# Performance work log

Measured on AMD Instinct MI355X. Metric: run time of the kernel, lower is better.

The kernel has to match this reference:

```python
import jax, jax.numpy as jnp
import numpy as np

N, T, F_IN, E, H, FW = 4096, 64, 8, 256, 512, 32
LN_EPS = 1e-5


def setup_inputs() -> dict:
    key = jax.random.key(0)
    ks = jax.random.split(key, 16)
    nrm = lambda k, s, sc=0.05: jax.random.normal(k, s, dtype=jnp.float32) * sc
    return {
        "x": nrm(ks[0], (N, T, F_IN), 1.0),
        "We": nrm(ks[1], (E, F_IN)), "be": nrm(ks[2], (E,)),
        "Wih0": nrm(ks[3], (4 * H, E)), "Whh0": nrm(ks[4], (4 * H, H)),
        "bih0": nrm(ks[5], (4 * H,)), "bhh0": nrm(ks[6], (4 * H,)),
        "Wih1": nrm(ks[7], (4 * H, H)), "Whh1": nrm(ks[8], (4 * H, H)),
        "bih1": nrm(ks[9], (4 * H,)), "bhh1": nrm(ks[10], (4 * H,)),
        "fc1_w": nrm(ks[11], (H, H)), "fc1_b": nrm(ks[12], (H,)),
        "ln_g": jnp.ones((H,), jnp.float32), "ln_b": jnp.zeros((H,), jnp.float32),
        "fc2_w": nrm(ks[13], (F_IN, H)), "fc2_b": nrm(ks[14], (F_IN,)),
    }


def _cell(x, h, c, Wih, Whh, bih, bhh):
    # PyTorch LSTM gate order: i, f, g, o
    g = x @ Wih.T + h @ Whh.T + (bih + bhh)
    i, f, gg, o = jnp.split(g, 4, axis=-1)
    c = jax.nn.sigmoid(f) * c + jax.nn.sigmoid(i) * jnp.tanh(gg)
    h = jax.nn.sigmoid(o) * jnp.tanh(c)
    return h, c


def _layer(xs, Wih, Whh, bih, bhh):
    # xs: (T, N, D) -> ys: (T, N, H), final (h, c)
    n = xs.shape[1]
    Hd = Whh.shape[1]
    h0 = jnp.zeros((n, Hd), xs.dtype)
    def step(carry, x_t):
        h, c = carry
        h, c = _cell(x_t, h, c, Wih, Whh, bih, bhh)
        return (h, c), h
    (h, c), ys = jax.lax.scan(step, (h0, h0), xs)
    return ys, h, c


def reference(x, We, be, Wih0, Whh0, bih0, bhh0, Wih1, Whh1, bih1, bhh1,
              fc1_w, fc1_b, ln_g, ln_b, fc2_w, fc2_b):
    x_enc = x[:, :-1, :]          # (N, T-1, F)
    x0 = x[:, -1, :]              # (N, F)

    # ---- encoder ----
    emb = x_enc @ We.T + be       # (N, T-1, E)
    xs = jnp.swapaxes(emb, 0, 1)  # (T-1, N, E)
    ys0, h0e, c0e = _layer(xs, Wih0, Whh0, bih0, bhh0)
    _, h1e, c1e = _layer(ys0, Wih1, Whh1, bih1, bhh1)

    # ---- decoder head: Linear -> LayerNorm -> ReLU -> Linear ----
    def fc(h):
        z = h @ fc1_w.T + fc1_b
        mu = z.mean(-1, keepdims=True)
        var = z.var(-1, keepdims=True)
        z = (z - mu) * jax.lax.rsqrt(var + LN_EPS) * ln_g + ln_b
        z = jax.nn.relu(z)
        return z @ fc2_w.T + fc2_b

    def dec_step(carry, _):
        xt, h0, c0, h1, c1 = carry
        e = xt @ We.T + be
        h0, c0 = _cell(e, h0, c0, Wih0, Whh0, bih0, bhh0)
        h1, c1 = _cell(h0, h1, c1, Wih1, Whh1, bih1, bhh1)
        y = fc(h1)
        return (y, h0, c0, h1, c1), y

    _, ys = jax.lax.scan(dec_step, (x0, h0e, c0e, h1e, c1e), None, length=FW)
    return jnp.swapaxes(ys, 0, 1)  # (N, FW, F)
```

## Files before the change

kernel.cpp:

```cpp
#include <hip/hip_runtime.h>
#include <math.h>

#define NB   4096
#define HID  512
#define G4H  2048
#define EDIM 256
#define FINP 8
#define TSTEPS 64
#define FWIN 32

typedef __bf16 bf16;
typedef bf16  bf16x8 __attribute__((ext_vector_type(8)));
typedef float f32x4  __attribute__((ext_vector_type(4)));

__device__ __forceinline__ float sigf(float x) { return 1.0f / (1.0f + __expf(-x)); }
__device__ __forceinline__ float tanhf_(float x) { return 2.0f * sigf(2.0f * x) - 1.0f; }

__device__ __forceinline__ void gload16(const void* g, void* l) {
    __builtin_amdgcn_global_load_lds((const __attribute__((address_space(1))) void*)g,
                                     (__attribute__((address_space(3))) void*)l, 16, 0, 0);
}

__device__ __forceinline__ void swz32(int& bx, int& by) {
    int nwg  = (int)(gridDim.x * gridDim.y);
    int orig = (int)(blockIdx.x + blockIdx.y * gridDim.x);
    int swz  = (orig & 7) * (nwg >> 3) + (orig >> 3);
    bx = swz & 31;
    by = swz >> 5;
}

__device__ __forceinline__ void gemm_acc(
    const bf16* __restrict__ A1, const bf16* __restrict__ W1,
    const bf16* __restrict__ A2, const bf16* __restrict__ W2, int npass,
    int m0, int n0, bf16 (&As)[2][4096], bf16 (&Ws)[2][4096], f32x4 (&acc)[4][4])
{
    const int tid  = threadIdx.x;
    const int lane = tid & 63;
    const int w    = tid >> 6;
    const int wr   = w >> 1, wc = w & 1;
    const int l16  = lane & 15;
    const int NK   = npass << 4;

    const int r0 = tid >> 2;
    const int o0 = ((tid & 3) ^ ((tid >> 3) & 3)) * 8;

    auto stage = [&](int s, int b) {
        const bf16* A = (s < 16) ? A1 : A2;
        const bf16* W = (s < 16) ? W1 : W2;
        const int k0 = ((s & 15) << 5) + o0;
        gload16(A + (size_t)(m0 + r0) * HID + k0,      &As[b][tid * 8]);
        gload16(A + (size_t)(m0 + r0 + 64) * HID + k0, &As[b][(tid + 256) * 8]);
        gload16(W + (size_t)(n0 + r0) * HID + k0,      &Ws[b][tid * 8]);
        gload16(W + (size_t)(n0 + r0 + 64) * HID + k0, &Ws[b][(tid + 256) * 8]);
    };

    const int swz_k = (((lane >> 4) ^ ((l16 >> 1) & 3))) * 8;
    const int aoff = wr * 2048 + l16 * 32 + swz_k;
    const int boff = wc * 2048 + l16 * 32 + swz_k;

    stage(0, 0);
    __syncthreads();
    int cur = 0;
    for (int s = 0; s < NK; ++s) {
        if (s + 1 < NK) stage(s + 1, cur ^ 1);
        const bf16* ap = &As[cur][aoff];
        const bf16* bp = &Ws[cur][boff];
        bf16x8 af[4], bfr[4];
#pragma unroll
        for (int m = 0; m < 4; ++m) af[m] = *(const bf16x8*)(ap + m * 512);
#pragma unroll
        for (int n = 0; n < 4; ++n) bfr[n] = *(const bf16x8*)(bp + n * 512);
#pragma unroll
        for (int m = 0; m < 4; ++m)
#pragma unroll
            for (int n = 0; n < 4; ++n)
                acc[m][n] = __builtin_amdgcn_mfma_f32_16x16x32_bf16(af[m], bfr[n], acc[m][n], 0, 0, 0);
        __syncthreads();
        cur ^= 1;
    }
}

template<bool HASX>
__device__ __forceinline__ void lstm_epi(f32x4 (&acc)[4][4],
    const float* __restrict__ Wfc, const float* __restrict__ bias,
    const float* __restrict__ xA, int sx,
    float* __restrict__ cst, bf16* __restrict__ hdst, int m0, int n0)
{
    const int tid = threadIdx.x, lane = tid & 63, w = tid >> 6;
    const int wr = w >> 1, wc = w & 1, l16 = lane & 15, lq = lane >> 4;
    const int hu = (n0 >> 2) + wc * 16 + l16;
    const int jb = n0 + wc * 64 + l16;

    float bq[4];
    f32x4 wf0[4], wf1[4];
#pragma unroll
    for (int g = 0; g < 4; ++g) {
        bq[g] = bias[jb + g * 16];
        if constexpr (HASX) {
            const float* wrow = Wfc + (size_t)(jb + g * 16) * 8;
            wf0[g] = *(const f32x4*)wrow;
            wf1[g] = *(const f32x4*)(wrow + 4);
        }
    }
#pragma unroll
    for (int m = 0; m < 4; ++m) {
        const int rb = m0 + wr * 64 + m * 16 + lq * 4;
#pragma unroll
        for (int q = 0; q < 4; ++q) {
            const int r = rb + q;
            float d0 = 0.f, d1 = 0.f, d2 = 0.f, d3 = 0.f;
            if constexpr (HASX) {
                const float* xr = xA + (size_t)r * sx;
                f32x4 xv0 = *(const f32x4*)xr;
                f32x4 xv1 = *(const f32x4*)(xr + 4);
                f32x4 p0 = xv0 * wf0[0] + xv1 * wf1[0];
                f32x4 p1 = xv0 * wf0[1] + xv1 * wf1[1];
                f32x4 p2 = xv0 * wf0[2] + xv1 * wf1[2];
                f32x4 p3 = xv0 * wf0[3] + xv1 * wf1[3];
                d0 = p0[0] + p0[1] + p0[2] + p0[3];
                d1 = p1[0] + p1[1] + p1[2] + p1[3];
                d2 = p2[0] + p2[1] + p2[2] + p2[3];
                d3 = p3[0] + p3[1] + p3[2] + p3[3];
            }
            float gi = acc[m][0][q] + bq[0] + d0;
            float gf = acc[m][1][q] + bq[1] + d1;
            float gg = acc[m][2][q] + bq[2] + d2;
            float go = acc[m][3][q] + bq[3] + d3;
            float iv = sigf(gi), fv = sigf(gf), gv = tanhf_(gg), ov = sigf(go);
            size_t ci = (size_t)r * HID + hu;
            float cn = fv * cst[ci] + iv * gv;
            cst[ci] = cn;
            hdst[ci] = (bf16)(ov * tanhf_(cn));
        }
    }
}

template<int NPASS, bool HASX>
__global__ __launch_bounds__(256)
void lstm_step(const bf16* __restrict__ A1, const bf16* __restrict__ W1,
               const bf16* __restrict__ A2, const bf16* __restrict__ W2,
               const float* __restrict__ Wfc, const float* __restrict__ bias,
               const float* __restrict__ xA, int sx,
               float* __restrict__ cst, bf16* __restrict__ hdst)
{
    __shared__ __align__(16) bf16 As[2][4096], Ws[2][4096];
    int bx, by; swz32(bx, by);
    const int m0 = bx * 128, n0 = by * 128;
    f32x4 acc[4][4];
#pragma unroll
    for (int m = 0; m < 4; ++m)
#pragma unroll
        for (int n = 0; n < 4; ++n) acc[m][n] = (f32x4){0.f, 0.f, 0.f, 0.f};
    gemm_acc(A1, W1, A2, W2, NPASS, m0, n0, As, Ws, acc);
    lstm_epi<HASX>(acc, Wfc, bias, xA, sx, cst, hdst, m0, n0);
}

template<bool L1TWO>
__global__ __launch_bounds__(256)
void enc_fused(const bf16* __restrict__ h0_in, const bf16* __restrict__ Whh0c,
               const float* __restrict__ Wf0c, const float* __restrict__ bf0c,
               const float* __restrict__ xA,
               bf16* __restrict__ h0_out, float* __restrict__ c0,
               const bf16* __restrict__ Wih1c, const bf16* __restrict__ h1_in,
               const bf16* __restrict__ Whh1c, const float* __restrict__ bs1c,
               bf16* __restrict__ h1_out, float* __restrict__ c1)
{
    __shared__ __align__(16) bf16 As[2][4096], Ws[2][4096];
    int orig = (int)(blockIdx.x + blockIdx.y * gridDim.x);
    int swz  = (orig & 7) * 128 + (orig >> 3);
    int layer = swz & 1;
    int rest  = swz >> 1;
    const int m0 = (rest & 31) * 128;
    const int n0 = (rest >> 5) * 128;
    f32x4 acc[4][4];
#pragma unroll
    for (int m = 0; m < 4; ++m)
#pragma unroll
        for (int n = 0; n < 4; ++n) acc[m][n] = (f32x4){0.f, 0.f, 0.f, 0.f};
    if (layer == 0) {
        gemm_acc(h0_in, Whh0c, nullptr, nullptr, 1, m0, n0, As, Ws, acc);
        lstm_epi<true>(acc, Wf0c, bf0c, xA, TSTEPS * FINP, c0, h0_out, m0, n0);
    } else {
        gemm_acc(h0_in, Wih1c, h1_in, Whh1c, L1TWO ? 2 : 1, m0, n0, As, Ws, acc);
        lstm_epi<false>(acc, nullptr, bs1c, nullptr, 0, c1, h1_out, m0, n0);
    }
}

__global__ __launch_bounds__(256)
void init_step(const float* __restrict__ x, const float* __restrict__ Wf0c,
               const float* __restrict__ bf0c, bf16* __restrict__ h0,
               float* __restrict__ c0)
{
    int idx = blockIdx.x * 256 + threadIdx.x;
    int r = idx >> 9, hu = idx & 511;
    const float* xr = x + (size_t)r * (TSTEPS * FINP);
    f32x4 xv0 = *(const f32x4*)xr;
    f32x4 xv1 = *(const f32x4*)(xr + 4);
    int jb = ((hu >> 4) << 6) + (hu & 15);
    float g[4];
#pragma unroll
    for (int gg = 0; gg < 4; ++gg) {
        const float* wrow = Wf0c + (size_t)(jb + gg * 16) * 8;
        f32x4 w0 = *(const f32x4*)wrow;
        f32x4 w1 = *(const f32x4*)(wrow + 4);
        f32x4 p = xv0 * w0 + xv1 * w1;
        g[gg] = bf0c[jb + gg * 16] + p[0] + p[1] + p[2] + p[3];
    }
    float iv = sigf(g[0]), gv = tanhf_(g[2]), ov = sigf(g[3]);
    float cn = iv * gv;
    c0[idx] = cn;
    h0[idx] = (bf16)(ov * tanhf_(cn));
}

__global__ __launch_bounds__(256)
void fc1_mfma(const bf16* __restrict__ A, const bf16* __restrict__ W,
              const float* __restrict__ bias, float* __restrict__ Z)
{
    __shared__ __align__(16) bf16 As[2][4096], Ws[2][4096];
    int bx, by; swz32(bx, by);
    const int m0 = bx * 128, n0 = by * 128;
    f32x4 acc[4][4];
#pragma unroll
    for (int m = 0; m < 4; ++m)
#pragma unroll
        for (int n = 0; n < 4; ++n) acc[m][n] = (f32x4){0.f, 0.f, 0.f, 0.f};
    gemm_acc(A, W, nullptr, nullptr, 1, m0, n0, As, Ws, acc);

    const int tid = threadIdx.x, lane = tid & 63, w = tid >> 6;
    const int wr = w >> 1, wc = w & 1, l16 = lane & 15, lq = lane >> 4;
#pragma unroll
    for (int m = 0; m < 4; ++m) {
        const int rb = m0 + wr * 64 + m * 16 + lq * 4;
#pragma unroll
        for (int n = 0; n < 4; ++n) {
            const int col = n0 + wc * 64 + n * 16 + l16;
            float bv = bias[col];
#pragma unroll
            for (int q = 0; q < 4; ++q)
                Z[(size_t)(rb + q) * HID + col] = acc[m][n][q] + bv;
        }
    }
}

__global__ __launch_bounds__(256)
void ln_fc2_kernel(const float* __restrict__ Z, const float* __restrict__ lng,
                   const float* __restrict__ lnb, const float* __restrict__ w2,
                   const float* __restrict__ b2, float* __restrict__ out)
{
    int wave = threadIdx.x >> 6;
    int lane = threadIdx.x & 63;
    int n = blockIdx.x * 4 + wave;
    const float* zr = Z + (size_t)n * HID;

    float v[8];
    float s1 = 0.f, s2 = 0.f;
#pragma unroll
    for (int j = 0; j < 8; ++j) {
        v[j] = zr[lane + j * 64];
        s1 += v[j];
        s2 += v[j] * v[j];
    }
#pragma unroll
    for (int off = 32; off; off >>= 1) {
        s1 += __shfl_down(s1, off);
        s2 += __shfl_down(s2, off);
    }
    s1 = __shfl(s1, 0);
    s2 = __shfl(s2, 0);
    float mu = s1 * (1.f / 512.f);
    float var = s2 * (1.f / 512.f) - mu * mu;
    float rs = rsqrtf(var + 1e-5f);

    float y[8];
#pragma unroll
    for (int f = 0; f < 8; ++f) y[f] = 0.f;
#pragma unroll
    for (int j = 0; j < 8; ++j) {
        int h = lane + j * 64;
        float zn = (v[j] - mu) * rs * lng[h] + lnb[h];
        zn = fmaxf(zn, 0.f);
#pragma unroll
        for (int f = 0; f < 8; ++f) y[f] += zn * w2[f * HID + h];
    }
#pragma unroll
    for (int f = 0; f < 8; ++f)
#pragma unroll
        for (int off = 32; off; off >>= 1) y[f] += __shfl_down(y[f], off);

    if (lane == 0) {
#pragma unroll
        for (int f = 0; f < 8; ++f) out[(size_t)n * 256 + f] = y[f] + b2[f];
    }
}

__device__ __forceinline__ int remap_j(int j) {
    int gate = j >> 9, hu = j & 511;
    return ((hu >> 4) << 6) + (gate << 4) + (hu & 15);
}

__global__ void fold_small(const float* __restrict__ Wih0, const float* __restrict__ We,
                           const float* __restrict__ be, const float* __restrict__ bih0,
                           const float* __restrict__ bhh0, const float* __restrict__ bih1,
                           const float* __restrict__ bhh1,
                           float* __restrict__ Wf0c, float* __restrict__ bf0c,
                           float* __restrict__ bs1c)
{
    int j = blockIdx.x * 256 + threadIdx.x;
    if (j >= G4H) return;
    int jn = remap_j(j);
    float acc[FINP];
#pragma unroll
    for (int f = 0; f < FINP; ++f) acc[f] = 0.f;
    float bacc = 0.f;
    for (int e = 0; e < EDIM; ++e) {
        float wv = Wih0[(size_t)j * EDIM + e];
        bacc += wv * be[e];
#pragma unroll
        for (int f = 0; f < FINP; ++f) acc[f] += wv * We[e * FINP + f];
    }
#pragma unroll
    for (int f = 0; f < FINP; ++f) Wf0c[(size_t)jn * FINP + f] = acc[f];
    bf0c[jn] = bacc + bih0[j] + bhh0[j];
    bs1c[jn] = bih1[j] + bhh1[j];
}

__global__ void conv_w(const float* __restrict__ W0, const float* __restrict__ W1,
                       const float* __restrict__ W2,
                       bf16* __restrict__ O0, bf16* __restrict__ O1, bf16* __restrict__ O2)
{
    int j = blockIdx.x;
    int which = blockIdx.y;
    const float* src = which == 0 ? W0 : which == 1 ? W1 : W2;
    bf16* dst = which == 0 ? O0 : which == 1 ? O1 : O2;
    int jn = remap_j(j);
    for (int k = threadIdx.x; k < HID; k += 256)
        dst[(size_t)jn * HID + k] = (bf16)src[(size_t)j * HID + k];
}

__global__ void conv_fc1(const float* __restrict__ W, bf16* __restrict__ O)
{
    int j = blockIdx.x;
    for (int k = threadIdx.x; k < HID; k += 256)
        O[(size_t)j * HID + k] = (bf16)W[(size_t)j * HID + k];
}

extern "C" void kernel_launch(void* const* d_in, const int* in_sizes, int n_in,
                              void* d_out, int out_size, void* d_ws, size_t ws_size,
                              hipStream_t stream)
{
    const float* x    = (const float*)d_in[0];
    const float* We   = (const float*)d_in[1];
    const float* be   = (const float*)d_in[2];
    const float* Wih0 = (const float*)d_in[3];
    const float* Whh0 = (const float*)d_in[4];
    const float* bih0 = (const float*)d_in[5];
    const float* bhh0 = (const float*)d_in[6];
    const float* Wih1 = (const float*)d_in[7];
    const float* Whh1 = (const float*)d_in[8];
    const float* bih1 = (const float*)d_in[9];
    const float* bhh1 = (const float*)d_in[10];
    const float* fc1w = (const float*)d_in[11];
    const float* fc1b = (const float*)d_in[12];
    const float* lng  = (const float*)d_in[13];
    const float* lnb  = (const float*)d_in[14];
    const float* fc2w = (const float*)d_in[15];
    const float* fc2b = (const float*)d_in[16];
    float* out = (float*)d_out;

    char* p = (char*)d_ws;
    auto alloc = [&](size_t bytes) -> void* {
        void* r = (void*)p;
        p += (bytes + 255) & ~(size_t)255;
        return r;
    };
    bf16*  Whh0c = (bf16*)alloc((size_t)G4H * HID * 2);
    bf16*  Wih1c = (bf16*)alloc((size_t)G4H * HID * 2);
    bf16*  Whh1c = (bf16*)alloc((size_t)G4H * HID * 2);
    bf16*  fc1wb = (bf16*)alloc((size_t)HID * HID * 2);
    float* Wf0c  = (float*)alloc((size_t)G4H * FINP * 4);
    float* bf0c  = (float*)alloc((size_t)G4H * 4);
    float* bs1c  = (float*)alloc((size_t)G4H * 4);
    const size_t S = (size_t)NB * HID;
    bf16*  H0[2]; H0[0] = (bf16*)alloc(S * 2); H0[1] = (bf16*)alloc(S * 2);
    bf16*  H1[2]; H1[0] = (bf16*)alloc(S * 2); H1[1] = (bf16*)alloc(S * 2);
    float* c0    = (float*)alloc(S * 4);
    float* c1    = (float*)alloc(S * 4);
    float* Z     = (float*)alloc(S * 4);

    hipMemsetAsync(c1, 0, S * 4, stream);

    fold_small<<<8, 256, 0, stream>>>(Wih0, We, be, bih0, bhh0, bih1, bhh1, Wf0c, bf0c, bs1c);
    conv_w<<<dim3(G4H, 3), 256, 0, stream>>>(Whh0, Wih1, Whh1, Whh0c, Wih1c, Whh1c);
    conv_fc1<<<HID, 256, 0, stream>>>(fc1w, fc1wb);

    init_step<<<NB * HID / 256, 256, 0, stream>>>(x, Wf0c, bf0c, H0[0], c0);

    dim3 fg(32, 32), lb(256);
    for (int t = 0; t < TSTEPS - 2; ++t) {
        if (t == 0)
            enc_fused<false><<<fg, lb, 0, stream>>>(H0[0], Whh0c, Wf0c, bf0c,
                x + (size_t)1 * FINP, H0[1], c0,
                Wih1c, nullptr, Whh1c, bs1c, H1[0], c1);
        else
            enc_fused<true><<<fg, lb, 0, stream>>>(H0[t & 1], Whh0c, Wf0c, bf0c,
                x + (size_t)(t + 1) * FINP, H0[(t + 1) & 1], c0,
                Wih1c, H1[(t + 1) & 1], Whh1c, bs1c, H1[t & 1], c1);
    }
    lstm_step<2, false><<<dim3(32, 16), lb, 0, stream>>>(
        H0[0], Wih1c, H1[1], Whh1c, nullptr, bs1c, nullptr, 0, c1, H1[0]);

    for (int s = 0; s < FWIN; ++s) {
        const float* xA = (s == 0) ? (x + (size_t)(TSTEPS - 1) * FINP)
                                   : (out + (size_t)(s - 1) * FINP);
        int sx = (s == 0) ? (TSTEPS * FINP) : (FWIN * FINP);
        lstm_step<1, true><<<dim3(32, 16), lb, 0, stream>>>(
            H0[s & 1], Whh0c, nullptr, nullptr, Wf0c, bf0c, xA, sx, c0, H0[(s + 1) & 1]);
        lstm_step<2, false><<<dim3(32, 16), lb, 0, stream>>>(
            H0[(s + 1) & 1], Wih1c, H1[s & 1], Whh1c, nullptr, bs1c, nullptr, 0,
            c1, H1[(s + 1) & 1]);
        fc1_mfma<<<dim3(32, 4), lb, 0, stream>>>(H1[(s + 1) & 1], fc1wb, fc1b, Z);
        ln_fc2_kernel<<<NB / 4, 256, 0, stream>>>(Z, lng, lnb, fc2w, fc2b,
                                                  out + (size_t)s * FINP);
    }
}
```

Before: 5.996 ms.

## Replace per-step encoder launches with a persistent cooperative kernel using per-group barriers

The 62 per-timestep encoder launches are replaced by one cooperative persistent kernel of 512 blocks. Each block owns a 128-row batch tile and a 128-column gate tile, and computes the layer-0 and then the layer-1 step for that tile. Only the 16 blocks sharing a batch tile synchronise, through an atomic counter barrier, so different batch groups can drift apart in time. This removes launch gaps and grid-wide step boundaries. In exchange, the two layers now run one after the other inside each block rather than concurrently across 1024 blocks. It also depends on every block being co-resident, and falls back to the old launch loop if the cooperative launch fails.

```diff
diff --git a/kernel.cpp b/kernel.cpp
--- a/kernel.cpp
+++ b/kernel.cpp
@@ -135,24 +135,57 @@
     }
 }
 
-template<int NPASS, bool HASX>
-__global__ __launch_bounds__(256)
-void lstm_step(const bf16* __restrict__ A1, const bf16* __restrict__ W1,
-               const bf16* __restrict__ A2, const bf16* __restrict__ W2,
-               const float* __restrict__ Wfc, const float* __restrict__ bias,
-               const float* __restrict__ xA, int sx,
-               float* __restrict__ cst, bf16* __restrict__ hdst)
+__device__ __forceinline__ void group_bar(unsigned* bar, int group, unsigned target) {
+    __syncthreads();
+    if (threadIdx.x == 0) {
+        __hip_atomic_fetch_add(&bar[group * 16], 1u, __ATOMIC_RELEASE, __HIP_MEMORY_SCOPE_AGENT);
+        while (__hip_atomic_load(&bar[group * 16], __ATOMIC_ACQUIRE, __HIP_MEMORY_SCOPE_AGENT) < target)
+            __builtin_amdgcn_s_sleep(1);
+    }
+    __syncthreads();
+}
+
+__global__ __launch_bounds__(256)
+void enc_persist2(bf16* H0a, bf16* H0b, bf16* H1a, bf16* H1b,
+                  const bf16* Whh0c, const bf16* Wih1c, const bf16* Whh1c,
+                  const float* Wf0c, const float* bf0c, const float* bs1c,
+                  const float* x, float* c0, float* c1, unsigned* bar)
 {
     __shared__ __align__(16) bf16 As[2][4096], Ws[2][4096];
-    int bx, by; swz32(bx, by);
-    const int m0 = bx * 128, n0 = by * 128;
+    const int gid   = (int)blockIdx.x;
+    const int group = gid >> 4;
+    const int role  = gid & 15;
+    const int m0    = group * 128;
+    const int n0    = role * 128;
+    bf16* H0[2] = {H0a, H0b};
+    bf16* H1[2] = {H1a, H1b};
+
     f32x4 acc[4][4];
+    for (int t = 0; t < TSTEPS - 2; ++t) {
+#pragma unroll
+        for (int m = 0; m < 4; ++m)
+#pragma unroll
+            for (int n = 0; n < 4; ++n) acc[m][n] = (f32x4){0.f, 0.f, 0.f, 0.f};
+        gemm_acc(H0[t & 1], Whh0c, nullptr, nullptr, 1, m0, n0, As, Ws, acc);
+        lstm_epi<true>(acc, Wf0c, bf0c, x + (size_t)(t + 1) * FINP, TSTEPS * FINP,
+                       c0, H0[(t + 1) & 1], m0, n0);
+#pragma unroll
+        for (int m = 0; m < 4; ++m)
+#pragma unroll
+            for (int n = 0; n < 4; ++n) acc[m][n] = (f32x4){0.f, 0.f, 0.f, 0.f};
+        if (t == 0)
+            gemm_acc(H0[0], Wih1c, nullptr, nullptr, 1, m0, n0, As, Ws, acc);
+        else
+            gemm_acc(H0[t & 1], Wih1c, H1[(t + 1) & 1], Whh1c, 2, m0, n0, As, Ws, acc);
+        lstm_epi<false>(acc, nullptr, bs1c, nullptr, 0, c1, H1[t & 1], m0, n0);
+        group_bar(bar, group, 16u * (t + 1));
+    }
 #pragma unroll
     for (int m = 0; m < 4; ++m)
 #pragma unroll
         for (int n = 0; n < 4; ++n) acc[m][n] = (f32x4){0.f, 0.f, 0.f, 0.f};
-    gemm_acc(A1, W1, A2, W2, NPASS, m0, n0, As, Ws, acc);
-    lstm_epi<HASX>(acc, Wfc, bias, xA, sx, cst, hdst, m0, n0);
+    gemm_acc(H0[0], Wih1c, H1[1], Whh1c, 2, m0, n0, As, Ws, acc);
+    lstm_epi<false>(acc, nullptr, bs1c, nullptr, 0, c1, H1[0], m0, n0);
 }
 
 template<bool L1TWO>
@@ -184,6 +217,26 @@
         gemm_acc(h0_in, Wih1c, h1_in, Whh1c, L1TWO ? 2 : 1, m0, n0, As, Ws, acc);
         lstm_epi<false>(acc, nullptr, bs1c, nullptr, 0, c1, h1_out, m0, n0);
     }
+}
+
+template<int NPASS, bool HASX>
+__global__ __launch_bounds__(256)
+void lstm_step(const bf16* __restrict__ A1, const bf16* __restrict__ W1,
+               const bf16* __restrict__ A2, const bf16* __restrict__ W2,
+               const float* __restrict__ Wfc, const float* __restrict__ bias,
+               const float* __restrict__ xA, int sx,
+               float* __restrict__ cst, bf16* __restrict__ hdst)
+{
+    __shared__ __align__(16) bf16 As[2][4096], Ws[2][4096];
+    int bx, by; swz32(bx, by);
+    const int m0 = bx * 128, n0 = by * 128;
+    f32x4 acc[4][4];
+#pragma unroll
+    for (int m = 0; m < 4; ++m)
+#pragma unroll
+        for (int n = 0; n < 4; ++n) acc[m][n] = (f32x4){0.f, 0.f, 0.f, 0.f};
+    gemm_acc(A1, W1, A2, W2, NPASS, m0, n0, As, Ws, acc);
+    lstm_epi<HASX>(acc, Wfc, bias, xA, sx, cst, hdst, m0, n0);
 }
 
 __global__ __launch_bounds__(256)
@@ -386,8 +439,10 @@
     float* c0    = (float*)alloc(S * 4);
     float* c1    = (float*)alloc(S * 4);
     float* Z     = (float*)alloc(S * 4);
+    unsigned* bar = (unsigned*)alloc(32 * 64);
 
     hipMemsetAsync(c1, 0, S * 4, stream);
+    hipMemsetAsync(bar, 0, 32 * 64, stream);
 
     fold_small<<<8, 256, 0, stream>>>(Wih0, We, be, bih0, bhh0, bih1, bhh1, Wf0c, bf0c, bs1c);
     conv_w<<<dim3(G4H, 3), 256, 0, stream>>>(Whh0, Wih1, Whh1, Whh0c, Wih1c, Whh1c);
@@ -395,19 +450,33 @@
 
     init_step<<<NB * HID / 256, 256, 0, stream>>>(x, Wf0c, bf0c, H0[0], c0);
 
-    dim3 fg(32, 32), lb(256);
-    for (int t = 0; t < TSTEPS - 2; ++t) {
-        if (t == 0)
-            enc_fused<false><<<fg, lb, 0, stream>>>(H0[0], Whh0c, Wf0c, bf0c,
-                x + (size_t)1 * FINP, H0[1], c0,
-                Wih1c, nullptr, Whh1c, bs1c, H1[0], c1);
-        else
-            enc_fused<true><<<fg, lb, 0, stream>>>(H0[t & 1], Whh0c, Wf0c, bf0c,
-                x + (size_t)(t + 1) * FINP, H0[(t + 1) & 1], c0,
-                Wih1c, H1[(t + 1) & 1], Whh1c, bs1c, H1[t & 1], c1);
-    }
-    lstm_step<2, false><<<dim3(32, 16), lb, 0, stream>>>(
-        H0[0], Wih1c, H1[1], Whh1c, nullptr, bs1c, nullptr, 0, c1, H1[0]);
+    dim3 lb(256);
+    {
+        bf16 *h0a = H0[0], *h0b = H0[1], *h1a = H1[0], *h1b = H1[1];
+        const float* xx = x;
+        void* args[] = {&h0a, &h0b, &h1a, &h1b,
+                        (void*)&Whh0c, (void*)&Wih1c, (void*)&Whh1c,
+                        (void*)&Wf0c, (void*)&bf0c, (void*)&bs1c,
+                        (void*)&xx, &c0, &c1, &bar};
+        hipError_t cerr = hipLaunchCooperativeKernel((const void*)enc_persist2,
+                                                     dim3(512), dim3(256), args, 0, stream);
+        if (cerr != hipSuccess) {
+            (void)hipGetLastError();
+            dim3 fg(32, 32);
+            for (int t = 0; t < TSTEPS - 2; ++t) {
+                if (t == 0)
+                    enc_fused<false><<<fg, lb, 0, stream>>>(H0[0], Whh0c, Wf0c, bf0c,
+                        x + (size_t)1 * FINP, H0[1], c0,
+                        Wih1c, nullptr, Whh1c, bs1c, H1[0], c1);
+                else
+                    enc_fused<true><<<fg, lb, 0, stream>>>(H0[t & 1], Whh0c, Wf0c, bf0c,
+                        x + (size_t)(t + 1) * FINP, H0[(t + 1) & 1], c0,
+                        Wih1c, H1[(t + 1) & 1], Whh1c, bs1c, H1[t & 1], c1);
+            }
+            lstm_step<2, false><<<dim3(32, 16), lb, 0, stream>>>(
+                H0[0], Wih1c, H1[1], Whh1c, nullptr, bs1c, nullptr, 0, c1, H1[0]);
+        }
+    }
 
     for (int s = 0; s < FWIN; ++s) {
         const float* xA = (s == 0) ? (x + (size_t)(TSTEPS - 1) * FINP)
```

Result: slower. 9.927 ms (+65.6%).
